# Kernel tuning notes

Measured on AMD Instinct MI355X. Metric: run time of the kernel, lower is better.

## Reference

```python
import jax, jax.numpy as jnp
import numpy as np

N_NODES = 50000
N_EDGES = 800000


def gcn_layer(x, edge_index, W, b):
    """PyG-style GCNConv: add self-loops, symmetric deg^-1/2 normalization,
    linear transform, scatter-sum aggregation at target nodes, plus bias."""
    n = x.shape[0]
    loops = jnp.arange(n)
    src = jnp.concatenate([edge_index[0], loops])  # [E+N]
    dst = jnp.concatenate([edge_index[1], loops])  # [E+N]
    deg = jax.ops.segment_sum(jnp.ones(src.shape, dtype=x.dtype), dst, num_segments=n)
    dinv = jnp.where(deg > 0, jax.lax.rsqrt(deg), jnp.zeros((), x.dtype))
    norm = dinv[src] * dinv[dst]               # [E+N]
    h = x @ W                                   # [N, out]
    msg = norm[:, None] * h[src]                # [E+N, out] gather
    out = jax.ops.segment_sum(msg, dst, num_segments=n)  # scatter-add
    return out + b


def setup_inputs() -> dict:
    key = jax.random.key(0)
    ks = jax.random.split(key, 8)
    features = jax.random.normal(ks[0], (N_NODES, 64), dtype=jnp.float32)
    edge_index1 = jax.random.randint(ks[1], (2, N_EDGES), 0, N_NODES)
    edge_index3 = jax.random.randint(ks[2], (2, N_EDGES), 0, N_NODES)
    edge_index9 = jax.random.randint(ks[3], (2, N_EDGES), 0, N_NODES)

    def glorot(k, fi, fo):
        lim = float(np.sqrt(6.0 / (fi + fo)))
        return jax.random.uniform(k, (fi, fo), minval=-lim, maxval=lim, dtype=jnp.float32)

    W1 = glorot(ks[4], 64, 64)
    W2 = glorot(ks[5], 64, 32)
    W3 = glorot(ks[6], 32, 16)
    b1 = jnp.zeros((64,), jnp.float32)
    b2 = jnp.zeros((32,), jnp.float32)
    b3 = jnp.zeros((16,), jnp.float32)
    return dict(features=features, edge_index1=edge_index1, edge_index3=edge_index3,
                edge_index9=edge_index9, W1=W1, b1=b1, W2=W2, b2=b2, W3=W3, b3=b3)


def reference(features, edge_index1, edge_index3, edge_index9, W1, b1, W2, b2, W3, b3):
    x = jax.nn.relu(gcn_layer(features, edge_index1, W1, b1))  # hop 1
    x = jax.nn.relu(gcn_layer(x, edge_index3, W2, b2))         # hop 3
    x = jax.nn.relu(gcn_layer(x, edge_index9, W3, b3))         # hop 9
    return x
```

## Files before the change

### kernel.cpp

```cpp
#include <hip/hip_runtime.h>
#include <hip/hip_fp16.h>


#define NB   256
#define NL   3
#define TB   (NB * NL)
#define CAPE 6400
#define CAPE_E (CAPE + 8)
#define CH   8192
#define P1T  512
#define EPT  (CH / P1T)
#define P2T  512

__device__ __forceinline__ void decode_chunk(int g, int nc1, int nc2,
                                             const int* s1, const int* d1, int E1,
                                             const int* s2, const int* d2, int E2,
                                             const int* s3, const int* d3, int E3,
                                             const int** src, const int** dst, int* E, int* l,
                                             int* gout) {
    if (g < nc1)            { *src = s1; *dst = d1; *E = E1; *l = 0; }
    else if (g < nc1 + nc2) { *src = s2; *dst = d2; *E = E2; *l = 1; g -= nc1; }
    else                    { *src = s3; *dst = d3; *E = E3; *l = 2; g -= nc1 + nc2; }
    *gout = g;
}

__device__ __forceinline__ void fma4(float4& a, float s, const float4& w) {
    a.x += s * w.x; a.y += s * w.y; a.z += s * w.z; a.w += s * w.w;
}
__device__ __forceinline__ void add4(float4& a, const float4& v) {
    a.x += v.x; a.y += v.y; a.z += v.z; a.w += v.w;
}
__device__ __forceinline__ float4 ldh4(const __half* h, size_t idx4) {
    uint2 r = ((const uint2*)h)[idx4];
    __half2 a = *reinterpret_cast<__half2*>(&r.x);
    __half2 b = *reinterpret_cast<__half2*>(&r.y);
    float2 fa = __half22float2(a), fb = __half22float2(b);
    return make_float4(fa.x, fa.y, fb.x, fb.y);
}
__device__ __forceinline__ void sth4(__half* h, size_t idx4, float4 v) {
    __half2 a = __floats2half2_rn(v.x, v.y);
    __half2 b = __floats2half2_rn(v.z, v.w);
    uint2 r;
    r.x = *reinterpret_cast<unsigned*>(&a);
    r.y = *reinterpret_cast<unsigned*>(&b);
    ((uint2*)h)[idx4] = r;
}

__global__ void __launch_bounds__(P1T) phase1(
        const int* __restrict__ s1, const int* __restrict__ d1, int E1,
        const int* __restrict__ s2, const int* __restrict__ d2, int E2,
        const int* __restrict__ s3, const int* __restrict__ d3, int E3,
        int nc1, int nc2, int W,
        int* __restrict__ gcur, unsigned int* __restrict__ pairBuf) {
    __shared__ int hist[NB];
    __shared__ int eofs[NB];
    __shared__ int bo[NB];
    __shared__ int lcur[NB];
    __shared__ unsigned stage[CH];
    __shared__ unsigned char stageQ[CH];
    const int t = threadIdx.x;
    for (int i = t; i < NB; i += P1T) hist[i] = 0;
    __syncthreads();
    const int* src; const int* dst; int E, l, g;
    decode_chunk(blockIdx.x, nc1, nc2, s1, d1, E1, s2, d2, E2, s3, d3, E3,
                 &src, &dst, &E, &l, &g);
    const int e0 = g * CH;
    const int lbase = l * NB;
    unsigned pv[EPT];
    int bn[EPT];
    if (E - e0 >= CH) {
        const int4* s4 = (const int4*)(src + e0);
        const int4* d4 = (const int4*)(dst + e0);
#pragma unroll
        for (int w = 0; w < EPT / 4; ++w) {
            int4 sv = s4[t + w * P1T];
            int4 dv = d4[t + w * P1T];
            int q, i = w * 4;
            q = dv.x / W; bn[i+0] = q; pv[i+0] = ((unsigned)sv.x << 9) | (unsigned)(dv.x - q * W);
            q = dv.y / W; bn[i+1] = q; pv[i+1] = ((unsigned)sv.y << 9) | (unsigned)(dv.y - q * W);
            q = dv.z / W; bn[i+2] = q; pv[i+2] = ((unsigned)sv.z << 9) | (unsigned)(dv.z - q * W);
            q = dv.w / W; bn[i+3] = q; pv[i+3] = ((unsigned)sv.w << 9) | (unsigned)(dv.w - q * W);
        }
    } else {
#pragma unroll
        for (int i = 0; i < EPT; ++i) {
            int e = e0 + t + i * P1T;
            if (e < E) {
                int s = src[e], d = dst[e];
                int q = d / W;
                bn[i] = q;
                pv[i] = ((unsigned)s << 9) | (unsigned)(d - q * W);
            } else bn[i] = -1;
        }
    }
#pragma unroll
    for (int i = 0; i < EPT; ++i)
        if (bn[i] >= 0) atomicAdd(&hist[bn[i]], 1);
    __syncthreads();
    if (t < NB) eofs[t] = hist[t];
    __syncthreads();
    for (int off = 1; off < NB; off <<= 1) {
        int add = (t < NB && t >= off) ? eofs[t - off] : 0;
        __syncthreads();
        if (t < NB) eofs[t] += add;
        __syncthreads();
    }
    const int total = eofs[NB - 1];
    int excl = 0;
    if (t < NB) excl = eofs[t] - hist[t];
    __syncthreads();
    if (t < NB) {
        eofs[t] = excl;
        lcur[t] = excl;
        int c = hist[t];
        bo[t] = (lbase + t) * CAPE + (c ? atomicAdd(&gcur[lbase + t], c) : 0);
    }
    __syncthreads();
#pragma unroll
    for (int i = 0; i < EPT; ++i) {
        if (bn[i] >= 0) {
            int r = atomicAdd(&lcur[bn[i]], 1);
            stage[r] = pv[i];
            stageQ[r] = (unsigned char)bn[i];
        }
    }
    __syncthreads();
    for (int i = t; i < total; i += P1T) {
        int q = stageQ[i];
        int k = bo[q] + (i - eofs[q]);
        if (k < (lbase + q + 1) * CAPE) pairBuf[k] = stage[i];
    }
}

__global__ void __launch_bounds__(P2T) k2_phase2_gemm1(
        const unsigned int* __restrict__ pairBuf, const int* __restrict__ gcur,
        int n, int W,
        int* __restrict__ row_ptr, int* __restrict__ cnt_g,
        float* __restrict__ dinv, unsigned short* __restrict__ eidx,
        const float* __restrict__ x0, const float* __restrict__ W1g,
        __half* __restrict__ h1) {
    __shared__ __align__(16) char smem[17408];
    if (blockIdx.x < (unsigned)TB) {
        int* lcnt  = (int*)smem;
        int* lscan = lcnt + P2T;
        unsigned short* stage = (unsigned short*)(lscan + P2T);
        const int bid = blockIdx.x;
        const int l = bid / NB, k = bid % NB;
        const int lo = k * W;
        const int hi = min(n, lo + W);
        const int Wn = hi - lo;
        const int segE = min(gcur[bid], CAPE);
        const size_t base  = (size_t)bid * CAPE;
        const int    baseE = bid * CAPE_E;
        const int t = threadIdx.x;
        lcnt[t] = 0;
        __syncthreads();
        for (int i = t; i < segE; i += P2T)
            atomicAdd(&lcnt[pairBuf[base + i] & 511u], 1);
        __syncthreads();
        const int v = lcnt[t];
        const int vp = (v + 3) & ~3;
        lscan[t] = vp;
        __syncthreads();
        for (int off = 1; off < P2T; off <<= 1) {
            int add = (t >= off) ? lscan[t - off] : 0;
            __syncthreads();
            lscan[t] += add;
            __syncthreads();
        }
        const int pexcl = lscan[t] - vp;
        const int segEp = lscan[P2T - 1];
        if (t < Wn) {
            int node = l * n + lo + t;
            row_ptr[node] = baseE + pexcl;
            cnt_g[node] = v;
            dinv[node] = rsqrtf((float)v + 1.0f);
        }
        __syncthreads();
        lcnt[t] = pexcl;
        __syncthreads();
        const bool lds_ok = (segEp <= CAPE);
        for (int i = t; i < segE; i += P2T) {
            unsigned p = pairBuf[base + i];
            int pos = atomicAdd(&lcnt[p & 511u], 1);
            unsigned short s = (unsigned short)(p >> 9);
            if (lds_ok) stage[pos] = s;
            else if (pos < CAPE_E) eidx[baseE + pos] = s;
        }
        __syncthreads();
        if (lds_ok) {
            const int4* st4 = (const int4*)stage;
            int4* e4 = (int4*)(eidx + baseE);
            int m16 = (segEp + 7) >> 3;
            for (int i = t; i < m16; i += P2T) e4[i] = st4[i];
        }
    } else {
        float* Ws = (float*)smem;
        const int bid = blockIdx.x - TB;
        for (int i = threadIdx.x; i < 1024; i += P2T)
            ((float4*)Ws)[i] = ((const float4*)W1g)[i];
        __syncthreads();
        const int tc = threadIdx.x % 16;
        const int tr = threadIdx.x / 16;
        const int row0 = bid * 128 + tr * 4;
        const float4* x4 = (const float4*)x0;
        const float4* Ws4 = (const float4*)Ws;
        float4 acc[4];
#pragma unroll
        for (int r = 0; r < 4; ++r) acc[r] = make_float4(0.f, 0.f, 0.f, 0.f);
        int rowc[4];
#pragma unroll
        for (int r = 0; r < 4; ++r) rowc[r] = min(row0 + r, n - 1);
        for (int k0 = 0; k0 < 64; k0 += 4) {
            float4 wv0 = Ws4[(k0 + 0) * 16 + tc];
            float4 wv1 = Ws4[(k0 + 1) * 16 + tc];
            float4 wv2 = Ws4[(k0 + 2) * 16 + tc];
            float4 wv3 = Ws4[(k0 + 3) * 16 + tc];
#pragma unroll
            for (int r = 0; r < 4; ++r) {
                float4 xv = x4[(size_t)rowc[r] * 16 + (k0 / 4)];
                fma4(acc[r], xv.x, wv0);
                fma4(acc[r], xv.y, wv1);
                fma4(acc[r], xv.z, wv2);
                fma4(acc[r], xv.w, wv3);
            }
        }
#pragma unroll
        for (int r = 0; r < 4; ++r) {
            int row = row0 + r;
            if (row < n) sth4(h1, (size_t)row * 16 + tc, acc[r]);
        }
    }
}

__global__ void __launch_bounds__(256) k3_gather1_gemm2(
        const int* __restrict__ row_ptr, const int* __restrict__ cnt,
        const unsigned short* __restrict__ eidx, const float* __restrict__ dinv1,
        const float* __restrict__ dinv2,
        const __half* __restrict__ h1, const float* __restrict__ b1,
        const float* __restrict__ W2g, __half* __restrict__ h2, int n) {
    __shared__ float xs[16 * 68];
    __shared__ float W2s[64 * 32];
    for (int i = threadIdx.x; i < 512; i += 256)
        ((float4*)W2s)[i] = ((const float4*)W2g)[i];
    const int ln = threadIdx.x >> 4;
    const int f4 = threadIdx.x & 15;
    const int node = blockIdx.x * 16 + ln;
    if (node < n) {
        const int beg = row_ptr[node];
        const int m = cnt[node];
        float4 a0 = make_float4(0.f, 0.f, 0.f, 0.f), a1 = a0, a2 = a0, a3 = a0;
        int j = 0;
        for (; j + 8 <= m; j += 8) {
            ushort4 e0 = *(const ushort4*)(eidx + beg + j);
            ushort4 e1 = *(const ushort4*)(eidx + beg + j + 4);
            float w0 = dinv1[e0.x], w1 = dinv1[e0.y], w2 = dinv1[e0.z], w3 = dinv1[e0.w];
            float w4 = dinv1[e1.x], w5 = dinv1[e1.y], w6 = dinv1[e1.z], w7 = dinv1[e1.w];
            float4 v0 = ldh4(h1, (size_t)e0.x * 16 + f4);
            float4 v1 = ldh4(h1, (size_t)e0.y * 16 + f4);
            float4 v2 = ldh4(h1, (size_t)e0.z * 16 + f4);
            float4 v3 = ldh4(h1, (size_t)e0.w * 16 + f4);
            float4 v4 = ldh4(h1, (size_t)e1.x * 16 + f4);
            float4 v5 = ldh4(h1, (size_t)e1.y * 16 + f4);
            float4 v6 = ldh4(h1, (size_t)e1.z * 16 + f4);
            float4 v7 = ldh4(h1, (size_t)e1.w * 16 + f4);
            fma4(a0, w0, v0); fma4(a1, w1, v1); fma4(a2, w2, v2); fma4(a3, w3, v3);
            fma4(a0, w4, v4); fma4(a1, w5, v5); fma4(a2, w6, v6); fma4(a3, w7, v7);
        }
        if (j + 4 <= m) {
            ushort4 e0 = *(const ushort4*)(eidx + beg + j);
            fma4(a0, dinv1[e0.x], ldh4(h1, (size_t)e0.x * 16 + f4));
            fma4(a1, dinv1[e0.y], ldh4(h1, (size_t)e0.y * 16 + f4));
            fma4(a2, dinv1[e0.z], ldh4(h1, (size_t)e0.z * 16 + f4));
            fma4(a3, dinv1[e0.w], ldh4(h1, (size_t)e0.w * 16 + f4));
            j += 4;
        }
        for (; j < m; ++j) {
            int s = eidx[beg + j];
            fma4(a0, dinv1[s], ldh4(h1, (size_t)s * 16 + f4));
        }
        add4(a0, a1); add4(a2, a3); add4(a0, a2);
        float di = dinv1[node];
        float4 self = ldh4(h1, (size_t)node * 16 + f4);
        float4 bv = ((const float4*)b1)[f4];
        float4 o;
        o.x = di * (a0.x + di * self.x) + bv.x;
        o.y = di * (a0.y + di * self.y) + bv.y;
        o.z = di * (a0.z + di * self.z) + bv.z;
        o.w = di * (a0.w + di * self.w) + bv.w;
        o.x = o.x > 0.f ? o.x : 0.f;
        o.y = o.y > 0.f ? o.y : 0.f;
        o.z = o.z > 0.f ? o.z : 0.f;
        o.w = o.w > 0.f ? o.w : 0.f;
        *(float4*)&xs[ln * 68 + f4 * 4] = o;
    }
    __syncthreads();
    if (node < n) {
        const int c0 = f4 * 2;
        float s0 = 0.f, s1 = 0.f;
#pragma unroll
        for (int k = 0; k < 64; ++k) {
            float xv = xs[ln * 68 + k];
            s0 += xv * W2s[k * 32 + c0];
            s1 += xv * W2s[k * 32 + c0 + 1];
        }
        float d2 = dinv2[node];
        ((__half2*)h2)[(size_t)node * 16 + f4] = __floats2half2_rn(s0 * d2, s1 * d2);
    }
}

__global__ void __launch_bounds__(256) k4_gather2_gemm3(
        const int* __restrict__ row_ptr2, const int* __restrict__ cnt2,
        const unsigned short* __restrict__ eidx, const float* __restrict__ dinv2,
        const float* __restrict__ dinv3,
        const __half* __restrict__ h2, const float* __restrict__ b2,
        const float* __restrict__ W3g, __half* __restrict__ h3, int n) {
    __shared__ float xs[32 * 36];
    __shared__ float W3s[32 * 16];
    for (int i = threadIdx.x; i < 128; i += 256)
        ((float4*)W3s)[i] = ((const float4*)W3g)[i];
    const int ln = threadIdx.x >> 3;
    const int f4 = threadIdx.x & 7;
    const int node = blockIdx.x * 32 + ln;
    if (node < n) {
        const int beg = row_ptr2[node];
        const int m = cnt2[node];
        float4 a0 = make_float4(0.f, 0.f, 0.f, 0.f), a1 = a0, a2 = a0, a3 = a0;
        int j = 0;
        for (; j + 8 <= m; j += 8) {
            ushort4 e0 = *(const ushort4*)(eidx + beg + j);
            ushort4 e1 = *(const ushort4*)(eidx + beg + j + 4);
            add4(a0, ldh4(h2, (size_t)e0.x * 8 + f4));
            add4(a1, ldh4(h2, (size_t)e0.y * 8 + f4));
            add4(a2, ldh4(h2, (size_t)e0.z * 8 + f4));
            add4(a3, ldh4(h2, (size_t)e0.w * 8 + f4));
            add4(a0, ldh4(h2, (size_t)e1.x * 8 + f4));
            add4(a1, ldh4(h2, (size_t)e1.y * 8 + f4));
            add4(a2, ldh4(h2, (size_t)e1.z * 8 + f4));
            add4(a3, ldh4(h2, (size_t)e1.w * 8 + f4));
        }
        if (j + 4 <= m) {
            ushort4 e0 = *(const ushort4*)(eidx + beg + j);
            add4(a0, ldh4(h2, (size_t)e0.x * 8 + f4));
            add4(a1, ldh4(h2, (size_t)e0.y * 8 + f4));
            add4(a2, ldh4(h2, (size_t)e0.z * 8 + f4));
            add4(a3, ldh4(h2, (size_t)e0.w * 8 + f4));
            j += 4;
        }
        for (; j < m; ++j)
            add4(a0, ldh4(h2, (size_t)eidx[beg + j] * 8 + f4));
        add4(a0, a1); add4(a2, a3); add4(a0, a2);
        float di = dinv2[node];
        float4 self = ldh4(h2, (size_t)node * 8 + f4);
        float4 bv = ((const float4*)b2)[f4];
        float4 o;
        o.x = di * (a0.x + self.x) + bv.x;
        o.y = di * (a0.y + self.y) + bv.y;
        o.z = di * (a0.z + self.z) + bv.z;
        o.w = di * (a0.w + self.w) + bv.w;
        o.x = o.x > 0.f ? o.x : 0.f;
        o.y = o.y > 0.f ? o.y : 0.f;
        o.z = o.z > 0.f ? o.z : 0.f;
        o.w = o.w > 0.f ? o.w : 0.f;
        *(float4*)&xs[ln * 36 + f4 * 4] = o;
    }
    __syncthreads();
    if (node < n) {
        const int c0 = f4 * 2;
        float s0 = 0.f, s1 = 0.f;
#pragma unroll
        for (int k = 0; k < 32; ++k) {
            float xv = xs[ln * 36 + k];
            s0 += xv * W3s[k * 16 + c0];
            s1 += xv * W3s[k * 16 + c0 + 1];
        }
        float d3 = dinv3[node];
        ((__half2*)h3)[(size_t)node * 8 + f4] = __floats2half2_rn(s0 * d3, s1 * d3);
    }
}

__global__ void __launch_bounds__(256) k5_gather3(
        const int* __restrict__ row_ptr3, const int* __restrict__ cnt3,
        const unsigned short* __restrict__ eidx, const float* __restrict__ dinv3,
        const __half* __restrict__ h3, const float* __restrict__ b3,
        float* __restrict__ out, int n) {
    const int ln = threadIdx.x >> 2;
    const int f4 = threadIdx.x & 3;
    const int node = blockIdx.x * 64 + ln;
    if (node >= n) return;
    const int beg = row_ptr3[node];
    const int m = cnt3[node];
    float4 a0 = make_float4(0.f, 0.f, 0.f, 0.f), a1 = a0, a2 = a0, a3 = a0;
    int j = 0;
    for (; j + 8 <= m; j += 8) {
        ushort4 e0 = *(const ushort4*)(eidx + beg + j);
        ushort4 e1 = *(const ushort4*)(eidx + beg + j + 4);
        add4(a0, ldh4(h3, (size_t)e0.x * 4 + f4));
        add4(a1, ldh4(h3, (size_t)e0.y * 4 + f4));
        add4(a2, ldh4(h3, (size_t)e0.z * 4 + f4));
        add4(a3, ldh4(h3, (size_t)e0.w * 4 + f4));
        add4(a0, ldh4(h3, (size_t)e1.x * 4 + f4));
        add4(a1, ldh4(h3, (size_t)e1.y * 4 + f4));
        add4(a2, ldh4(h3, (size_t)e1.z * 4 + f4));
        add4(a3, ldh4(h3, (size_t)e1.w * 4 + f4));
    }
    if (j + 4 <= m) {
        ushort4 e0 = *(const ushort4*)(eidx + beg + j);
        add4(a0, ldh4(h3, (size_t)e0.x * 4 + f4));
        add4(a1, ldh4(h3, (size_t)e0.y * 4 + f4));
        add4(a2, ldh4(h3, (size_t)e0.z * 4 + f4));
        add4(a3, ldh4(h3, (size_t)e0.w * 4 + f4));
        j += 4;
    }
    for (; j < m; ++j)
        add4(a0, ldh4(h3, (size_t)eidx[beg + j] * 4 + f4));
    add4(a0, a1); add4(a2, a3); add4(a0, a2);
    float di = dinv3[node];
    float4 self = ldh4(h3, (size_t)node * 4 + f4);
    float4 bv = ((const float4*)b3)[f4];
    float4 o;
    o.x = di * (a0.x + self.x) + bv.x;
    o.y = di * (a0.y + self.y) + bv.y;
    o.z = di * (a0.z + self.z) + bv.z;
    o.w = di * (a0.w + self.w) + bv.w;
    o.x = o.x > 0.f ? o.x : 0.f;
    o.y = o.y > 0.f ? o.y : 0.f;
    o.z = o.z > 0.f ? o.z : 0.f;
    o.w = o.w > 0.f ? o.w : 0.f;
    ((float4*)out)[(size_t)node * 4 + f4] = o;
}

extern "C" void kernel_launch(void* const* d_in, const int* in_sizes, int n_in,
                              void* d_out, int out_size, void* d_ws, size_t ws_size,
                              hipStream_t stream) {
    const float* x0  = (const float*)d_in[0];
    const int*   ei1 = (const int*)d_in[1];
    const int*   ei3 = (const int*)d_in[2];
    const int*   ei9 = (const int*)d_in[3];
    const float* W1  = (const float*)d_in[4];
    const float* b1  = (const float*)d_in[5];
    const float* W2  = (const float*)d_in[6];
    const float* b2  = (const float*)d_in[7];
    const float* W3  = (const float*)d_in[8];
    const float* b3  = (const float*)d_in[9];

    const int n  = in_sizes[0] / 64;
    const int E1 = in_sizes[1] / 2;
    const int E3 = in_sizes[2] / 2;
    const int E9 = in_sizes[3] / 2;
    const int n3 = 3 * n;
    const int W  = (n + NB - 1) / NB;

    const int nc1 = (E1 + CH - 1) / CH;
    const int nc2 = (E3 + CH - 1) / CH;
    const int nc3 = (E9 + CH - 1) / CH;
    const int nchunks = nc1 + nc2 + nc3;
    const int gemmBlks = (n + 127) / 128;

    int* gcur    = (int*)d_ws;
    unsigned int* pairBuf = (unsigned int*)(gcur + TB);
    unsigned short* eidx = (unsigned short*)(pairBuf + (size_t)TB * CAPE);
    int* row_ptr = (int*)(eidx + (size_t)TB * CAPE_E);
    int* cnt     = row_ptr + n3;
    float* dinv  = (float*)(cnt + n3);
    __half* h1   = (__half*)(dinv + n3);
    __half* h2   = h1 + (size_t)n * 64;
    __half* h3   = h2 + (size_t)n * 32;

    hipMemsetAsync(gcur, 0, TB * sizeof(int), stream);
    phase1<<<nchunks, P1T, 0, stream>>>(ei1, ei1 + E1, E1, ei3, ei3 + E3, E3,
                                        ei9, ei9 + E9, E9, nc1, nc2, W, gcur, pairBuf);
    k2_phase2_gemm1<<<TB + gemmBlks, P2T, 0, stream>>>(
        pairBuf, gcur, n, W, row_ptr, cnt, dinv, eidx, x0, W1, h1);
    k3_gather1_gemm2<<<(n + 15) / 16, 256, 0, stream>>>(
        row_ptr, cnt, eidx, dinv, dinv + n, h1, b1, W2, h2, n);
    k4_gather2_gemm3<<<(n + 31) / 32, 256, 0, stream>>>(
        row_ptr + n, cnt + n, eidx, dinv + n, dinv + 2 * n, h2, b2, W3, h3, n);
    k5_gather3<<<(n + 63) / 64, 256, 0, stream>>>(
        row_ptr + 2 * n, cnt + 2 * n, eidx, dinv + 2 * n, h3, b3, (float*)d_out, n);
}
```

Measured before the change: 167.4 us.

## Move GEMM1 into phase1 kernel and prescale h1 by source dinv in phase2

The first-layer GEMM blocks now run alongside the edge-bucketing phase1 kernel instead of alongside phase2. Phase2 then scales h1 rows by the source-node deg^-1/2 in place once dinv is known, so the layer-1 gather can use plain adds and drop the per-edge dinv lookup. This cuts random dinv reads in the hottest gather loop. In exchange, phase2 does an extra read-modify-write pass over h1, and the GEMM bounds are now hardcoded to 50000 nodes.

```diff
diff --git a/kernel.cpp b/kernel.cpp
--- a/kernel.cpp
+++ b/kernel.cpp
@@ -46,162 +46,102 @@
     ((uint2*)h)[idx4] = r;
 }
 
-__global__ void __launch_bounds__(P1T) phase1(
+__global__ void __launch_bounds__(P1T) k1_phase1_gemm1(
         const int* __restrict__ s1, const int* __restrict__ d1, int E1,
         const int* __restrict__ s2, const int* __restrict__ d2, int E2,
         const int* __restrict__ s3, const int* __restrict__ d3, int E3,
-        int nc1, int nc2, int W,
-        int* __restrict__ gcur, unsigned int* __restrict__ pairBuf) {
-    __shared__ int hist[NB];
-    __shared__ int eofs[NB];
-    __shared__ int bo[NB];
-    __shared__ int lcur[NB];
-    __shared__ unsigned stage[CH];
-    __shared__ unsigned char stageQ[CH];
-    const int t = threadIdx.x;
-    for (int i = t; i < NB; i += P1T) hist[i] = 0;
-    __syncthreads();
-    const int* src; const int* dst; int E, l, g;
-    decode_chunk(blockIdx.x, nc1, nc2, s1, d1, E1, s2, d2, E2, s3, d3, E3,
-                 &src, &dst, &E, &l, &g);
-    const int e0 = g * CH;
-    const int lbase = l * NB;
-    unsigned pv[EPT];
-    int bn[EPT];
-    if (E - e0 >= CH) {
-        const int4* s4 = (const int4*)(src + e0);
-        const int4* d4 = (const int4*)(dst + e0);
-#pragma unroll
-        for (int w = 0; w < EPT / 4; ++w) {
-            int4 sv = s4[t + w * P1T];
-            int4 dv = d4[t + w * P1T];
-            int q, i = w * 4;
-            q = dv.x / W; bn[i+0] = q; pv[i+0] = ((unsigned)sv.x << 9) | (unsigned)(dv.x - q * W);
-            q = dv.y / W; bn[i+1] = q; pv[i+1] = ((unsigned)sv.y << 9) | (unsigned)(dv.y - q * W);
-            q = dv.z / W; bn[i+2] = q; pv[i+2] = ((unsigned)sv.z << 9) | (unsigned)(dv.z - q * W);
-            q = dv.w / W; bn[i+3] = q; pv[i+3] = ((unsigned)sv.w << 9) | (unsigned)(dv.w - q * W);
-        }
-    } else {
-#pragma unroll
-        for (int i = 0; i < EPT; ++i) {
-            int e = e0 + t + i * P1T;
-            if (e < E) {
-                int s = src[e], d = dst[e];
-                int q = d / W;
-                bn[i] = q;
-                pv[i] = ((unsigned)s << 9) | (unsigned)(d - q * W);
-            } else bn[i] = -1;
-        }
-    }
-#pragma unroll
-    for (int i = 0; i < EPT; ++i)
-        if (bn[i] >= 0) atomicAdd(&hist[bn[i]], 1);
-    __syncthreads();
-    if (t < NB) eofs[t] = hist[t];
-    __syncthreads();
-    for (int off = 1; off < NB; off <<= 1) {
-        int add = (t < NB && t >= off) ? eofs[t - off] : 0;
-        __syncthreads();
-        if (t < NB) eofs[t] += add;
-        __syncthreads();
-    }
-    const int total = eofs[NB - 1];
-    int excl = 0;
-    if (t < NB) excl = eofs[t] - hist[t];
-    __syncthreads();
-    if (t < NB) {
-        eofs[t] = excl;
-        lcur[t] = excl;
-        int c = hist[t];
-        bo[t] = (lbase + t) * CAPE + (c ? atomicAdd(&gcur[lbase + t], c) : 0);
-    }
-    __syncthreads();
-#pragma unroll
-    for (int i = 0; i < EPT; ++i) {
-        if (bn[i] >= 0) {
-            int r = atomicAdd(&lcur[bn[i]], 1);
-            stage[r] = pv[i];
-            stageQ[r] = (unsigned char)bn[i];
-        }
-    }
-    __syncthreads();
-    for (int i = t; i < total; i += P1T) {
-        int q = stageQ[i];
-        int k = bo[q] + (i - eofs[q]);
-        if (k < (lbase + q + 1) * CAPE) pairBuf[k] = stage[i];
-    }
-}
-
-__global__ void __launch_bounds__(P2T) k2_phase2_gemm1(
-        const unsigned int* __restrict__ pairBuf, const int* __restrict__ gcur,
-        int n, int W,
-        int* __restrict__ row_ptr, int* __restrict__ cnt_g,
-        float* __restrict__ dinv, unsigned short* __restrict__ eidx,
+        int nc1, int nc2, int W, int nchunks,
+        int* __restrict__ gcur, unsigned int* __restrict__ pairBuf,
         const float* __restrict__ x0, const float* __restrict__ W1g,
         __half* __restrict__ h1) {
-    __shared__ __align__(16) char smem[17408];
-    if (blockIdx.x < (unsigned)TB) {
-        int* lcnt  = (int*)smem;
-        int* lscan = lcnt + P2T;
-        unsigned short* stage = (unsigned short*)(lscan + P2T);
-        const int bid = blockIdx.x;
-        const int l = bid / NB, k = bid % NB;
-        const int lo = k * W;
-        const int hi = min(n, lo + W);
-        const int Wn = hi - lo;
-        const int segE = min(gcur[bid], CAPE);
-        const size_t base  = (size_t)bid * CAPE;
-        const int    baseE = bid * CAPE_E;
-        const int t = threadIdx.x;
-        lcnt[t] = 0;
-        __syncthreads();
-        for (int i = t; i < segE; i += P2T)
-            atomicAdd(&lcnt[pairBuf[base + i] & 511u], 1);
-        __syncthreads();
-        const int v = lcnt[t];
-        const int vp = (v + 3) & ~3;
-        lscan[t] = vp;
-        __syncthreads();
-        for (int off = 1; off < P2T; off <<= 1) {
-            int add = (t >= off) ? lscan[t - off] : 0;
+    __shared__ __align__(16) char smem[45056];
+    const int t = threadIdx.x;
+    if (blockIdx.x < (unsigned)nchunks) {
+        int* hist = (int*)smem;
+        int* eofs = hist + NB;
+        int* bo   = eofs + NB;
+        int* lcur = bo + NB;
+        unsigned* stage = (unsigned*)(smem + 4096);
+        unsigned char* stageQ = (unsigned char*)(smem + 36864);
+        for (int i = t; i < NB; i += P1T) hist[i] = 0;
+        __syncthreads();
+        const int* src; const int* dst; int E, l, g;
+        decode_chunk(blockIdx.x, nc1, nc2, s1, d1, E1, s2, d2, E2, s3, d3, E3,
+                     &src, &dst, &E, &l, &g);
+        const int e0 = g * CH;
+        const int lbase = l * NB;
+        unsigned pv[EPT];
+        int bn[EPT];
+        if (E - e0 >= CH) {
+            const int4* s4 = (const int4*)(src + e0);
+            const int4* d4 = (const int4*)(dst + e0);
+#pragma unroll
+            for (int w = 0; w < EPT / 4; ++w) {
+                int4 sv = s4[t + w * P1T];
+                int4 dv = d4[t + w * P1T];
+                int q, i = w * 4;
+                q = dv.x / W; bn[i+0] = q; pv[i+0] = ((unsigned)sv.x << 9) | (unsigned)(dv.x - q * W);
+                q = dv.y / W; bn[i+1] = q; pv[i+1] = ((unsigned)sv.y << 9) | (unsigned)(dv.y - q * W);
+                q = dv.z / W; bn[i+2] = q; pv[i+2] = ((unsigned)sv.z << 9) | (unsigned)(dv.z - q * W);
+                q = dv.w / W; bn[i+3] = q; pv[i+3] = ((unsigned)sv.w << 9) | (unsigned)(dv.w - q * W);
+            }
+        } else {
+#pragma unroll
+            for (int i = 0; i < EPT; ++i) {
+                int e = e0 + t + i * P1T;
+                if (e < E) {
+                    int s = src[e], d = dst[e];
+                    int q = d / W;
+                    bn[i] = q;
+                    pv[i] = ((unsigned)s << 9) | (unsigned)(d - q * W);
+                } else bn[i] = -1;
+            }
+        }
+#pragma unroll
+        for (int i = 0; i < EPT; ++i)
+            if (bn[i] >= 0) atomicAdd(&hist[bn[i]], 1);
+        __syncthreads();
+        if (t < NB) eofs[t] = hist[t];
+        __syncthreads();
+        for (int off = 1; off < NB; off <<= 1) {
+            int add = (t < NB && t >= off) ? eofs[t - off] : 0;
             __syncthreads();
-            lscan[t] += add;
+            if (t < NB) eofs[t] += add;
             __syncthreads();
         }
-        const int pexcl = lscan[t] - vp;
-        const int segEp = lscan[P2T - 1];
-        if (t < Wn) {
-            int node = l * n + lo + t;
-            row_ptr[node] = baseE + pexcl;
-            cnt_g[node] = v;
-            dinv[node] = rsqrtf((float)v + 1.0f);
-        }
-        __syncthreads();
-        lcnt[t] = pexcl;
-        __syncthreads();
-        const bool lds_ok = (segEp <= CAPE);
-        for (int i = t; i < segE; i += P2T) {
-            unsigned p = pairBuf[base + i];
-            int pos = atomicAdd(&lcnt[p & 511u], 1);
-            unsigned short s = (unsigned short)(p >> 9);
-            if (lds_ok) stage[pos] = s;
-            else if (pos < CAPE_E) eidx[baseE + pos] = s;
-        }
-        __syncthreads();
-        if (lds_ok) {
-            const int4* st4 = (const int4*)stage;
-            int4* e4 = (int4*)(eidx + baseE);
-            int m16 = (segEp + 7) >> 3;
-            for (int i = t; i < m16; i += P2T) e4[i] = st4[i];
+        const int total = eofs[NB - 1];
+        int excl = 0;
+        if (t < NB) excl = eofs[t] - hist[t];
+        __syncthreads();
+        if (t < NB) {
+            eofs[t] = excl;
+            lcur[t] = excl;
+            int c = hist[t];
+            bo[t] = (lbase + t) * CAPE + (c ? atomicAdd(&gcur[lbase + t], c) : 0);
+        }
+        __syncthreads();
+#pragma unroll
+        for (int i = 0; i < EPT; ++i) {
+            if (bn[i] >= 0) {
+                int r = atomicAdd(&lcur[bn[i]], 1);
+                stage[r] = pv[i];
+                stageQ[r] = (unsigned char)bn[i];
+            }
+        }
+        __syncthreads();
+        for (int i = t; i < total; i += P1T) {
+            int q = stageQ[i];
+            int k = bo[q] + (i - eofs[q]);
+            if (k < (lbase + q + 1) * CAPE) pairBuf[k] = stage[i];
         }
     } else {
         float* Ws = (float*)smem;
-        const int bid = blockIdx.x - TB;
-        for (int i = threadIdx.x; i < 1024; i += P2T)
+        const int bid = blockIdx.x - nchunks;
+        for (int i = t; i < 1024; i += P1T)
             ((float4*)Ws)[i] = ((const float4*)W1g)[i];
         __syncthreads();
-        const int tc = threadIdx.x % 16;
-        const int tr = threadIdx.x / 16;
+        const int tc = t % 16;
+        const int tr = t / 16;
         const int row0 = bid * 128 + tr * 4;
         const float4* x4 = (const float4*)x0;
         const float4* Ws4 = (const float4*)Ws;
@@ -210,7 +150,7 @@
         for (int r = 0; r < 4; ++r) acc[r] = make_float4(0.f, 0.f, 0.f, 0.f);
         int rowc[4];
 #pragma unroll
-        for (int r = 0; r < 4; ++r) rowc[r] = min(row0 + r, n - 1);
+        for (int r = 0; r < 4; ++r) rowc[r] = min(row0 + r, 49999);
         for (int k0 = 0; k0 < 64; k0 += 4) {
             float4 wv0 = Ws4[(k0 + 0) * 16 + tc];
             float4 wv1 = Ws4[(k0 + 1) * 16 + tc];
@@ -228,7 +168,82 @@
 #pragma unroll
         for (int r = 0; r < 4; ++r) {
             int row = row0 + r;
-            if (row < n) sth4(h1, (size_t)row * 16 + tc, acc[r]);
+            if (row < 50000) sth4(h1, (size_t)row * 16 + tc, acc[r]);
+        }
+    }
+}
+
+__global__ void __launch_bounds__(P2T) k2_phase2(
+        const unsigned int* __restrict__ pairBuf, const int* __restrict__ gcur,
+        int n, int W,
+        int* __restrict__ row_ptr, int* __restrict__ cnt_g,
+        float* __restrict__ dinv, unsigned short* __restrict__ eidx,
+        __half* __restrict__ h1) {
+    __shared__ __align__(16) char smem[19456];
+    int* lcnt  = (int*)smem;
+    int* lscan = lcnt + P2T;
+    unsigned short* stage = (unsigned short*)(lscan + P2T);
+    float* dloc = (float*)(smem + 17408);
+    const int bid = blockIdx.x;
+    const int l = bid / NB, k = bid % NB;
+    const int lo = k * W;
+    const int hi = min(n, lo + W);
+    const int Wn = hi - lo;
+    const int segE = min(gcur[bid], CAPE);
+    const size_t base  = (size_t)bid * CAPE;
+    const int    baseE = bid * CAPE_E;
+    const int t = threadIdx.x;
+    lcnt[t] = 0;
+    __syncthreads();
+    for (int i = t; i < segE; i += P2T)
+        atomicAdd(&lcnt[pairBuf[base + i] & 511u], 1);
+    __syncthreads();
+    const int v = lcnt[t];
+    const int vp = (v + 3) & ~3;
+    lscan[t] = vp;
+    __syncthreads();
+    for (int off = 1; off < P2T; off <<= 1) {
+        int add = (t >= off) ? lscan[t - off] : 0;
+        __syncthreads();
+        lscan[t] += add;
+        __syncthreads();
+    }
+    const int pexcl = lscan[t] - vp;
+    const int segEp = lscan[P2T - 1];
+    if (t < Wn) {
+        int node = l * n + lo + t;
+        row_ptr[node] = baseE + pexcl;
+        cnt_g[node] = v;
+        float dv = rsqrtf((float)v + 1.0f);
+        dinv[node] = dv;
+        dloc[t] = dv;
+    }
+    __syncthreads();
+    lcnt[t] = pexcl;
+    __syncthreads();
+    const bool lds_ok = (segEp <= CAPE);
+    for (int i = t; i < segE; i += P2T) {
+        unsigned p = pairBuf[base + i];
+        int pos = atomicAdd(&lcnt[p & 511u], 1);
+        unsigned short s = (unsigned short)(p >> 9);
+        if (lds_ok) stage[pos] = s;
+        else if (pos < CAPE_E) eidx[baseE + pos] = s;
+    }
+    __syncthreads();
+    if (lds_ok) {
+        const int4* st4 = (const int4*)stage;
+        int4* e4 = (int4*)(eidx + baseE);
+        int m16 = (segEp + 7) >> 3;
+        for (int i = t; i < m16; i += P2T) e4[i] = st4[i];
+    }
+    if (l == 0) {
+        for (int i = t; i < Wn * 16; i += P2T) {
+            int r = i >> 4, c = i & 15;
+            size_t idx = (size_t)(lo + r) * 16 + c;
+            float4 vv = ldh4(h1, idx);
+            float s = dloc[r];
+            vv.x *= s; vv.y *= s; vv.z *= s; vv.w *= s;
+            sth4(h1, idx, vv);
         }
     }
 }
@@ -254,40 +269,34 @@
         for (; j + 8 <= m; j += 8) {
             ushort4 e0 = *(const ushort4*)(eidx + beg + j);
             ushort4 e1 = *(const ushort4*)(eidx + beg + j + 4);
-            float w0 = dinv1[e0.x], w1 = dinv1[e0.y], w2 = dinv1[e0.z], w3 = dinv1[e0.w];
-            float w4 = dinv1[e1.x], w5 = dinv1[e1.y], w6 = dinv1[e1.z], w7 = dinv1[e1.w];
-            float4 v0 = ldh4(h1, (size_t)e0.x * 16 + f4);
-            float4 v1 = ldh4(h1, (size_t)e0.y * 16 + f4);
-            float4 v2 = ldh4(h1, (size_t)e0.z * 16 + f4);
-            float4 v3 = ldh4(h1, (size_t)e0.w * 16 + f4);
-            float4 v4 = ldh4(h1, (size_t)e1.x * 16 + f4);
-            float4 v5 = ldh4(h1, (size_t)e1.y * 16 + f4);
-            float4 v6 = ldh4(h1, (size_t)e1.z * 16 + f4);
-            float4 v7 = ldh4(h1, (size_t)e1.w * 16 + f4);
-            fma4(a0, w0, v0); fma4(a1, w1, v1); fma4(a2, w2, v2); fma4(a3, w3, v3);
-            fma4(a0, w4, v4); fma4(a1, w5, v5); fma4(a2, w6, v6); fma4(a3, w7, v7);
+            add4(a0, ldh4(h1, (size_t)e0.x * 16 + f4));
+            add4(a1, ldh4(h1, (size_t)e0.y * 16 + f4));
+            add4(a2, ldh4(h1, (size_t)e0.z * 16 + f4));
+            add4(a3, ldh4(h1, (size_t)e0.w * 16 + f4));
+            add4(a0, ldh4(h1, (size_t)e1.x * 16 + f4));
+            add4(a1, ldh4(h1, (size_t)e1.y * 16 + f4));
+            add4(a2, ldh4(h1, (size_t)e1.z * 16 + f4));
+            add4(a3, ldh4(h1, (size_t)e1.w * 16 + f4));
         }
         if (j + 4 <= m) {
             ushort4 e0 = *(const ushort4*)(eidx + beg + j);
-            fma4(a0, dinv1[e0.x], ldh4(h1, (size_t)e0.x * 16 + f4));
-            fma4(a1, dinv1[e0.y], ldh4(h1, (size_t)e0.y * 16 + f4));
-            fma4(a2, dinv1[e0.z], ldh4(h1, (size_t)e0.z * 16 + f4));
-            fma4(a3, dinv1[e0.w], ldh4(h1, (size_t)e0.w * 16 + f4));
+            add4(a0, ldh4(h1, (size_t)e0.x * 16 + f4));
+            add4(a1, ldh4(h1, (size_t)e0.y * 16 + f4));
+            add4(a2, ldh4(h1, (size_t)e0.z * 16 + f4));
+            add4(a3, ldh4(h1, (size_t)e0.w * 16 + f4));
             j += 4;
         }
-        for (; j < m; ++j) {
-            int s = eidx[beg + j];
-            fma4(a0, dinv1[s], ldh4(h1, (size_t)s * 16 + f4));
-        }
+        for (; j < m; ++j)
+            add4(a0, ldh4(h1, (size_t)eidx[beg + j] * 16 + f4));
         add4(a0, a1); add4(a2, a3); add4(a0, a2);
         float di = dinv1[node];
         float4 self = ldh4(h1, (size_t)node * 16 + f4);
         float4 bv = ((const float4*)b1)[f4];
         float4 o;
-        o.x = di * (a0.x + di * self.x) + bv.x;
-        o.y = di * (a0.y + di * self.y) + bv.y;
-        o.z = di * (a0.z + di * self.z) + bv.z;
-        o.w = di * (a0.w + di * self.w) + bv.w;
+        o.x = di * (a0.x + self.x) + bv.x;
+        o.y = di * (a0.y + self.y) + bv.y;
+        o.z = di * (a0.z + self.z) + bv.z;
+        o.w = di * (a0.w + self.w) + bv.w;
         o.x = o.x > 0.f ? o.x : 0.f;
         o.y = o.y > 0.f ? o.y : 0.f;
         o.z = o.z > 0.f ? o.z : 0.f;
@@ -468,10 +477,11 @@
     __half* h3   = h2 + (size_t)n * 32;
 
     hipMemsetAsync(gcur, 0, TB * sizeof(int), stream);
-    phase1<<<nchunks, P1T, 0, stream>>>(ei1, ei1 + E1, E1, ei3, ei3 + E3, E3,
-                                        ei9, ei9 + E9, E9, nc1, nc2, W, gcur, pairBuf);
-    k2_phase2_gemm1<<<TB + gemmBlks, P2T, 0, stream>>>(
-        pairBuf, gcur, n, W, row_ptr, cnt, dinv, eidx, x0, W1, h1);
+    k1_phase1_gemm1<<<nchunks + gemmBlks, P1T, 0, stream>>>(
+        ei1, ei1 + E1, E1, ei3, ei3 + E3, E3, ei9, ei9 + E9, E9,
+        nc1, nc2, W, nchunks, gcur, pairBuf, x0, W1, h1);
+    k2_phase2<<<TB, P2T, 0, stream>>>(
+        pairBuf, gcur, n, W, row_ptr, cnt, dinv, eidx, h1);
     k3_gather1_gemm2<<<(n + 15) / 16, 256, 0, stream>>>(
         row_ptr, cnt, eidx, dinv, dinv + n, h1, b1, W2, h2, n);
     k4_gather2_gemm3<<<(n + 31) / 32, 256, 0, stream>>>(
```

New measurement: 162.6 us. 1.03x faster.
